# Kernel tuning notes

Measured on AMD Instinct MI355X. Metric: run time of the kernel, lower is better.

Reference implementation:

```python
import jax, jax.numpy as jnp
import numpy as np

B, S, D_IN, D_OUT = 4, 2048, 1024, 1024


def setup_inputs() -> dict:
    key = jax.random.key(0)
    kx, kq, kk, kv = jax.random.split(key, 4)
    scale = 1.0 / np.sqrt(D_IN)
    return {
        "x": jax.random.normal(kx, (B, S, D_IN), dtype=jnp.float32),
        "W_q": jax.random.normal(kq, (D_IN, D_OUT), dtype=jnp.float32) * scale,
        "W_k": jax.random.normal(kk, (D_IN, D_OUT), dtype=jnp.float32) * scale,
        "W_v": jax.random.normal(kv, (D_IN, D_OUT), dtype=jnp.float32) * scale,
    }


def reference(x, W_q, W_k, W_v):
    # QKV projections (Linear without bias): [B,S,D_out]
    q = jnp.einsum("bsd,de->bse", x, W_q)
    k = jnp.einsum("bsd,de->bse", x, W_k)
    v = jnp.einsum("bsd,de->bse", x, W_v)

    # Raw scores [B,S,S], causal mask (strict upper triangle -> -inf),
    # then scale by sqrt(d_k) and softmax, matching the torch order of ops.
    scores = jnp.einsum("bqd,bkd->bqk", q, k)
    seq = scores.shape[-1]
    causal = jnp.triu(jnp.ones((seq, seq), dtype=bool), k=1)
    scores = jnp.where(causal[None, :, :], -jnp.inf, scores)
    attn = jax.nn.softmax(scores / jnp.sqrt(jnp.asarray(q.shape[-1], scores.dtype)), axis=-1)
    # dropout p=0.0 -> identity (eval semantics)
    return jnp.einsum("bqk,bkd->bqd", attn, v)
```

## Files before the change

### kernel.cpp

```cpp
#include <hip/hip_runtime.h>

typedef unsigned short u16;
typedef __bf16 bf16x8 __attribute__((ext_vector_type(8)));
typedef float f32x4 __attribute__((ext_vector_type(4)));

__device__ __forceinline__ u16 f2bf(float f) {
    union { float f; unsigned int u; } v; v.f = f;
    unsigned int u = v.u;
    return (u16)((u + 0x7FFFu + ((u >> 16) & 1u)) >> 16);
}

__device__ __forceinline__ void load_lds16(const void* g, void* l) {
    __builtin_amdgcn_global_load_lds(
        (const __attribute__((address_space(1))) unsigned int*)g,
        (__attribute__((address_space(3))) unsigned int*)l,
        16, 0, 0);
}

__global__ void __launch_bounds__(256) prep_kernel(
    const float4* __restrict__ X, u16* __restrict__ xb,
    const float* __restrict__ Wq, const float* __restrict__ Wk,
    const float* __restrict__ Wv,
    u16* __restrict__ Oq, u16* __restrict__ Ok, u16* __restrict__ Ov,
    float* __restrict__ rowsum) {
    __shared__ float tile[32][33];
    const int bid = blockIdx.x, tid = threadIdx.x;
    if (bid < 8192) {
        int idx = bid * 256 + tid;
        float4 v = X[idx];
        ushort4 o;
        o.x = f2bf(v.x); o.y = f2bf(v.y); o.z = f2bf(v.z); o.w = f2bf(v.w);
        *(ushort4*)(xb + (size_t)idx * 4) = o;
    } else if (bid < 11264) {
        int id = bid - 8192;
        int zz = id >> 10;
        const float* W = (zz == 0) ? Wq : (zz == 1) ? Wk : Wv;
        u16* O = (zz == 0) ? Oq : (zz == 1) ? Ok : Ov;
        int n0 = (id & 31) * 32, k0 = ((id >> 5) & 31) * 32;
        int tx = tid & 31, ty = tid >> 5;
        #pragma unroll
        for (int j = 0; j < 32; j += 8)
            tile[ty + j][tx] = W[(size_t)(k0 + ty + j) * 1024 + n0 + tx];
        __syncthreads();
        #pragma unroll
        for (int j = 0; j < 32; j += 8)
            O[(size_t)(n0 + ty + j) * 1024 + k0 + tx] = f2bf(tile[tx][ty + j]);
    } else {
        rowsum[(bid - 11264) * 256 + tid] = 0.f;
    }
}

template <int MODE>
__global__ void __launch_bounds__(512) gemm_nt(
    const u16* __restrict__ xb, const u16* __restrict__ WqT,
    const u16* __restrict__ WkT, const u16* __restrict__ WvT,
    u16* __restrict__ Q, u16* __restrict__ Kb,
    u16* __restrict__ Vt, u16* __restrict__ S,
    float* __restrict__ rowsum, float* __restrict__ out) {

    int mtile, ntile, z, kiters;
    const u16 *A, *B;

    if (MODE == 0) {
        int L = blockIdx.x;
        int xcd = L & 7;
        int u = L >> 3;
        z = u >> 5;
        int v = u & 31;
        mtile = ((v >> 3) << 3) | xcd;
        ntile = v & 7;
        A = xb;
        B = (z == 0) ? WqT : (z == 1) ? WkT : WvT;
        kiters = 16;
    } else if (MODE == 1) {
        int L = blockIdx.x;
        z = L >> 7;
        int w = L & 127;
        mtile = w >> 4;
        ntile = w & 15;
        if (ntile > 2 * mtile + 1) return;
        A = Q  + (size_t)z * (2048 * 1024);
        B = Kb + (size_t)z * (2048 * 1024);
        kiters = 16;
    } else {
        int L = blockIdx.x;
        ntile = L & 7;
        int mt = L >> 3;
        z = mt >> 3;
        mtile = mt & 7;
        A = S  + (size_t)z * (2048 * 2048);
        B = Vt + (size_t)z * (1024 * 2048);
        kiters = 4 * (mtile + 1);
    }

    const int LDA = (MODE == 2) ? 2048 : 1024;

    __shared__ __align__(16) u16 As[32768];
    __shared__ __align__(16) u16 Bs[16384 + MODE * 128];

    const int tid  = threadIdx.x;
    const int lane = tid & 63;
    const int wave = tid >> 6;
    const int wr = wave >> 1, wc = wave & 1;

    const int r0 = tid >> 2;
    const int kb = (((tid & 3) ^ ((r0 >> 1) & 3))) * 16;

    const char* gA0 = (const char*)(A + (size_t)(mtile * 256 +       r0) * LDA) + kb;
    const char* gA1 = (const char*)(A + (size_t)(mtile * 256 + 128 + r0) * LDA) + kb;
    const char* gB  = (const char*)(B + (size_t)(ntile * 128 +       r0) * LDA) + kb;

    auto STAGE = [&](int buf, int kt) {
        const size_t off = (size_t)kt * 128;
        char* a = (char*)As + buf * 32768 + tid * 16;
        char* b = (char*)Bs + buf * 16384 + tid * 16;
        load_lds16(gA0 + off,      a);
        load_lds16(gA0 + off + 64, a + 8192);
        load_lds16(gA1 + off,      a + 16384);
        load_lds16(gA1 + off + 64, a + 24576);
        load_lds16(gB  + off,      b);
        load_lds16(gB  + off + 64, b + 8192);
    };

    const int quad = lane >> 4;
    const int l16  = lane & 15;
    const int ch   = quad ^ ((l16 >> 1) & 3);
    const int aoff = (wr >> 1) * 8192 + ((wr & 1) * 64 + l16) * 32 + ch * 8;
    const int boff = (wc * 64 + l16) * 32 + ch * 8;

    f32x4 acc[4][4] = {};

    STAGE(0, 0);
    STAGE(1, 1);
    asm volatile("s_waitcnt vmcnt(6)" ::: "memory");
    __builtin_amdgcn_s_barrier();

    int cur = 0;
    for (int kt = 0; kt < kiters; ++kt) {
        const u16* ap = As + cur * 16384 + aoff;
        const u16* bp = Bs + cur * 8192  + boff;
        bf16x8 af[2][4], bv[2][4];
        #pragma unroll
        for (int h = 0; h < 2; ++h) {
            #pragma unroll
            for (int r = 0; r < 4; ++r) af[h][r] = *(const bf16x8*)(ap + h * 4096 + r * 512);
            #pragma unroll
            for (int c = 0; c < 4; ++c) bv[h][c] = *(const bf16x8*)(bp + h * 4096 + c * 512);
        }
        asm volatile("s_waitcnt lgkmcnt(0)" ::: "memory");
        __builtin_amdgcn_sched_barrier(0);
        __builtin_amdgcn_s_barrier();
        if (kt + 2 < kiters) STAGE(cur, kt + 2);

        #pragma unroll
        for (int h = 0; h < 2; ++h)
            #pragma unroll
            for (int r = 0; r < 4; ++r)
                #pragma unroll
                for (int c = 0; c < 4; ++c)
                    acc[r][c] = __builtin_amdgcn_mfma_f32_16x16x32_bf16(
                        af[h][r], bv[h][c], acc[r][c], 0, 0, 0);

        if (kt + 2 < kiters) {
            asm volatile("s_waitcnt vmcnt(6)" ::: "memory");
        } else {
            asm volatile("s_waitcnt vmcnt(0)" ::: "memory");
        }
        __builtin_amdgcn_s_barrier();
        cur ^= 1;
    }

    const int grow0 = mtile * 256 + wr * 64 + quad * 4;
    const int gcol0 = ntile * 128 + wc * 64 + l16;

    if (MODE == 0) {
        if (z < 2) {
            u16* C = z ? Kb : Q;
            #pragma unroll
            for (int r = 0; r < 4; ++r)
                #pragma unroll
                for (int c = 0; c < 4; ++c)
                    #pragma unroll
                    for (int i = 0; i < 4; ++i)
                        C[(size_t)(grow0 + r * 16 + i) * 1024 + gcol0 + c * 16] =
                            f2bf(acc[r][c][i]);
        } else {
            #pragma unroll
            for (int r = 0; r < 4; ++r) {
                int m0 = grow0 + r * 16;
                int b = m0 >> 11, s0 = m0 & 2047;
                #pragma unroll
                for (int c = 0; c < 4; ++c) {
                    int d = gcol0 + c * 16;
                    ushort4 o;
                    o.x = f2bf(acc[r][c][0]); o.y = f2bf(acc[r][c][1]);
                    o.z = f2bf(acc[r][c][2]); o.w = f2bf(acc[r][c][3]);
                    *(ushort4*)(Vt + (size_t)b * (1024 * 2048) + (size_t)d * 2048 + s0) = o;
                }
            }
        }
    } else if (MODE == 1) {
        u16* C = S + (size_t)z * (2048 * 2048);
        float* rs = rowsum + z * 2048;
        const bool maskchk = (ntile >= 2 * mtile);
        float rsum[4][4];
        #pragma unroll
        for (int r = 0; r < 4; ++r)
            #pragma unroll
            for (int i = 0; i < 4; ++i) rsum[r][i] = 0.f;
        #pragma unroll
        for (int r = 0; r < 4; ++r)
            #pragma unroll
            for (int c = 0; c < 4; ++c)
                #pragma unroll
                for (int i = 0; i < 4; ++i) {
                    int grow = grow0 + r * 16 + i;
                    int gcol = gcol0 + c * 16;
                    float e = 0.f;
                    if (!maskchk || gcol <= grow)
                        e = __expf(acc[r][c][i] * 0.03125f - 12.0f);
                    C[(size_t)grow * 2048 + gcol] = f2bf(e);
                    rsum[r][i] += e;
                }
        #pragma unroll
        for (int r = 0; r < 4; ++r)
            #pragma unroll
            for (int i = 0; i < 4; ++i) {
                float s = rsum[r][i];
                s += __shfl_xor(s, 1, 64);
                s += __shfl_xor(s, 2, 64);
                s += __shfl_xor(s, 4, 64);
                s += __shfl_xor(s, 8, 64);
                if (l16 == 0)
                    unsafeAtomicAdd(&rs[grow0 + r * 16 + i], s);
            }
    } else {
        const float* rs = rowsum + z * 2048;
        float* C = out + (size_t)z * (2048 * 1024);
        #pragma unroll
        for (int r = 0; r < 4; ++r)
            #pragma unroll
            for (int i = 0; i < 4; ++i) {
                int grow = grow0 + r * 16 + i;
                float inv = 1.0f / rs[grow];
                #pragma unroll
                for (int c = 0; c < 4; ++c)
                    C[(size_t)grow * 1024 + gcol0 + c * 16] = acc[r][c][i] * inv;
            }
    }
}

extern "C" void kernel_launch(void* const* d_in, const int* in_sizes, int n_in,
                              void* d_out, int out_size, void* d_ws, size_t ws_size,
                              hipStream_t stream) {
    const float* x  = (const float*)d_in[0];
    const float* Wq = (const float*)d_in[1];
    const float* Wk = (const float*)d_in[2];
    const float* Wv = (const float*)d_in[3];
    float* out = (float*)d_out;
    char* ws = (char*)d_ws;
    const size_t Mi = 1u << 20;

    u16* xb  = (u16*)(ws);
    u16* WqT = (u16*)(ws + 16 * Mi);
    u16* WkT = (u16*)(ws + 18 * Mi);
    u16* WvT = (u16*)(ws + 20 * Mi);
    u16* Q   = (u16*)(ws + 22 * Mi);
    u16* Kb  = (u16*)(ws + 38 * Mi);
    u16* Vt  = (u16*)(ws + 54 * Mi);
    u16* S   = (u16*)(ws + 70 * Mi);
    float* rowsum = (float*)(ws + 102 * Mi);

    prep_kernel<<<11296, 256, 0, stream>>>(
        (const float4*)x, xb, Wq, Wk, Wv, WqT, WkT, WvT, rowsum);

    gemm_nt<0><<<768, 512, 0, stream>>>(xb, WqT, WkT, WvT, Q, Kb, Vt, S, rowsum, out);

    gemm_nt<1><<<512, 512, 0, stream>>>(xb, WqT, WkT, WvT, Q, Kb, Vt, S, rowsum, out);

    gemm_nt<2><<<256, 512, 0, stream>>>(xb, WqT, WkT, WvT, Q, Kb, Vt, S, rowsum, out);
}
```

Before: 232.7 us.

## Split-K heavy PV tiles into halves and software-pipeline LDS fragment loads

The PV GEMM (mode 2) used one block per output tile, with K length growing with mtile, so the causal workload was badly imbalanced. The longest row tiles (mtile 5-7) are now split into two K halves. One half writes unnormalized partials to a scratch buffer that reuses the xb region, and a new combine kernel sums the halves and applies the row normalization. The main loop is also restructured to double-buffer LDS fragment reads across k sub-steps, with s_setprio around the MFMA groups, so LDS reads overlap matrix math. This costs an extra kernel launch and extra fp32 global traffic for the partials.

```diff
diff --git a/kernel.cpp b/kernel.cpp
--- a/kernel.cpp
+++ b/kernel.cpp
@@ -16,6 +16,9 @@
         (__attribute__((address_space(3))) unsigned int*)l,
         16, 0, 0);
 }
+
+__constant__ unsigned char cls2_m[11] = {4,7,7,3,6,6,5,5,2,1,0};
+__constant__ unsigned char cls2_h[11] = {2,0,1,2,0,1,0,1,2,2,2};
 
 __global__ void __launch_bounds__(256) prep_kernel(
     const float4* __restrict__ X, u16* __restrict__ xb,
@@ -50,15 +53,35 @@
     }
 }
 
+__global__ void __launch_bounds__(256) combine_kernel(
+    const float4* __restrict__ P1, const float* __restrict__ rowsum,
+    float4* __restrict__ out) {
+    int b = blockIdx.x;
+    int z = b / 768;
+    int lb = b - z * 768;
+    int j = lb * 256 + threadIdx.x;
+    int rl = j >> 8;
+    float inv = 1.0f / rowsum[z * 2048 + 1280 + rl];
+    size_t oi = (size_t)z * 524288 + 327680 + j;
+    float4 a = out[oi];
+    float4 p = P1[(size_t)z * 196608 + j];
+    a.x = (a.x + p.x) * inv;
+    a.y = (a.y + p.y) * inv;
+    a.z = (a.z + p.z) * inv;
+    a.w = (a.w + p.w) * inv;
+    out[oi] = a;
+}
+
 template <int MODE>
 __global__ void __launch_bounds__(512) gemm_nt(
     const u16* __restrict__ xb, const u16* __restrict__ WqT,
     const u16* __restrict__ WkT, const u16* __restrict__ WvT,
     u16* __restrict__ Q, u16* __restrict__ Kb,
     u16* __restrict__ Vt, u16* __restrict__ S,
-    float* __restrict__ rowsum, float* __restrict__ out) {
-
-    int mtile, ntile, z, kiters;
+    float* __restrict__ rowsum, float* __restrict__ out,
+    float* __restrict__ P1) {
+
+    int mtile, ntile, z, kbeg = 0, kiters, kh = 2;
     const u16 *A, *B;
 
     if (MODE == 0) {
@@ -85,12 +108,16 @@
     } else {
         int L = blockIdx.x;
         ntile = L & 7;
-        int mt = L >> 3;
-        z = mt >> 3;
-        mtile = mt & 7;
+        z = (L >> 3) & 3;
+        int ci = L >> 5;
+        mtile = cls2_m[ci];
+        kh = cls2_h[ci];
+        int half = 2 * (mtile + 1);
+        if (kh == 0)      { kbeg = 0;    kiters = half; }
+        else if (kh == 1) { kbeg = half; kiters = half; }
+        else              { kbeg = 0;    kiters = 4 * (mtile + 1); }
         A = S  + (size_t)z * (2048 * 2048);
         B = Vt + (size_t)z * (1024 * 2048);
-        kiters = 4 * (mtile + 1);
     }
 
     const int LDA = (MODE == 2) ? 2048 : 1024;
@@ -106,12 +133,12 @@
     const int r0 = tid >> 2;
     const int kb = (((tid & 3) ^ ((r0 >> 1) & 3))) * 16;
 
-    const char* gA0 = (const char*)(A + (size_t)(mtile * 256 +       r0) * LDA) + kb;
-    const char* gA1 = (const char*)(A + (size_t)(mtile * 256 + 128 + r0) * LDA) + kb;
-    const char* gB  = (const char*)(B + (size_t)(ntile * 128 +       r0) * LDA) + kb;
-
-    auto STAGE = [&](int buf, int kt) {
-        const size_t off = (size_t)kt * 128;
+    const char* gA0 = (const char*)(A + (size_t)(mtile * 256 +       r0) * LDA) + kb + kbeg * 128;
+    const char* gA1 = (const char*)(A + (size_t)(mtile * 256 + 128 + r0) * LDA) + kb + kbeg * 128;
+    const char* gB  = (const char*)(B + (size_t)(ntile * 128 +       r0) * LDA) + kb + kbeg * 128;
+
+    auto STAGE = [&](int buf, int kt2) {
+        const size_t off = (size_t)kt2 * 128;
         char* a = (char*)As + buf * 32768 + tid * 16;
         char* b = (char*)Bs + buf * 16384 + tid * 16;
         load_lds16(gA0 + off,      a);
@@ -129,44 +156,67 @@
     const int boff = (wc * 64 + l16) * 32 + ch * 8;
 
     f32x4 acc[4][4] = {};
+    bf16x8 afA[4], bvA[4], afB[4], bvB[4];
 
     STAGE(0, 0);
     STAGE(1, 1);
     asm volatile("s_waitcnt vmcnt(6)" ::: "memory");
     __builtin_amdgcn_s_barrier();
+    {
+        const u16* ap = As + aoff;
+        const u16* bp = Bs + boff;
+        #pragma unroll
+        for (int r = 0; r < 4; ++r) afA[r] = *(const bf16x8*)(ap + r * 512);
+        #pragma unroll
+        for (int c = 0; c < 4; ++c) bvA[c] = *(const bf16x8*)(bp + c * 512);
+    }
 
     int cur = 0;
     for (int kt = 0; kt < kiters; ++kt) {
-        const u16* ap = As + cur * 16384 + aoff;
-        const u16* bp = Bs + cur * 8192  + boff;
-        bf16x8 af[2][4], bv[2][4];
-        #pragma unroll
-        for (int h = 0; h < 2; ++h) {
-            #pragma unroll
-            for (int r = 0; r < 4; ++r) af[h][r] = *(const bf16x8*)(ap + h * 4096 + r * 512);
-            #pragma unroll
-            for (int c = 0; c < 4; ++c) bv[h][c] = *(const bf16x8*)(bp + h * 4096 + c * 512);
+        {
+            const u16* ap = As + cur * 16384 + 4096 + aoff;
+            const u16* bp = Bs + cur * 8192  + 4096 + boff;
+            #pragma unroll
+            for (int r = 0; r < 4; ++r) afB[r] = *(const bf16x8*)(ap + r * 512);
+            #pragma unroll
+            for (int c = 0; c < 4; ++c) bvB[c] = *(const bf16x8*)(bp + c * 512);
         }
+        asm volatile("s_waitcnt lgkmcnt(8)" ::: "memory");
+        __builtin_amdgcn_sched_barrier(0);
+        __builtin_amdgcn_s_setprio(1);
+        #pragma unroll
+        for (int r = 0; r < 4; ++r)
+            #pragma unroll
+            for (int c = 0; c < 4; ++c)
+                acc[r][c] = __builtin_amdgcn_mfma_f32_16x16x32_bf16(
+                    afA[r], bvA[c], acc[r][c], 0, 0, 0);
+        __builtin_amdgcn_s_setprio(0);
         asm volatile("s_waitcnt lgkmcnt(0)" ::: "memory");
         __builtin_amdgcn_sched_barrier(0);
         __builtin_amdgcn_s_barrier();
         if (kt + 2 < kiters) STAGE(cur, kt + 2);
-
-        #pragma unroll
-        for (int h = 0; h < 2; ++h)
-            #pragma unroll
-            for (int r = 0; r < 4; ++r)
-                #pragma unroll
-                for (int c = 0; c < 4; ++c)
-                    acc[r][c] = __builtin_amdgcn_mfma_f32_16x16x32_bf16(
-                        af[h][r], bv[h][c], acc[r][c], 0, 0, 0);
-
-        if (kt + 2 < kiters) {
-            asm volatile("s_waitcnt vmcnt(6)" ::: "memory");
-        } else {
-            asm volatile("s_waitcnt vmcnt(0)" ::: "memory");
+        if (kt + 1 < kiters) {
+            if (kt + 2 < kiters) {
+                asm volatile("s_waitcnt vmcnt(6)" ::: "memory");
+            } else {
+                asm volatile("s_waitcnt vmcnt(0)" ::: "memory");
+            }
+            __builtin_amdgcn_s_barrier();
+            const u16* ap = As + (cur ^ 1) * 16384 + aoff;
+            const u16* bp = Bs + (cur ^ 1) * 8192  + boff;
+            #pragma unroll
+            for (int r = 0; r < 4; ++r) afA[r] = *(const bf16x8*)(ap + r * 512);
+            #pragma unroll
+            for (int c = 0; c < 4; ++c) bvA[c] = *(const bf16x8*)(bp + c * 512);
         }
-        __builtin_amdgcn_s_barrier();
+        __builtin_amdgcn_s_setprio(1);
+        #pragma unroll
+        for (int r = 0; r < 4; ++r)
+            #pragma unroll
+            for (int c = 0; c < 4; ++c)
+                acc[r][c] = __builtin_amdgcn_mfma_f32_16x16x32_bf16(
+                    afB[r], bvB[c], acc[r][c], 0, 0, 0);
+        __builtin_amdgcn_s_setprio(0);
         cur ^= 1;
     }
 
@@ -235,18 +285,42 @@
                     unsafeAtomicAdd(&rs[grow0 + r * 16 + i], s);
             }
     } else {
-        const float* rs = rowsum + z * 2048;
-        float* C = out + (size_t)z * (2048 * 1024);
-        #pragma unroll
-        for (int r = 0; r < 4; ++r)
-            #pragma unroll
-            for (int i = 0; i < 4; ++i) {
-                int grow = grow0 + r * 16 + i;
-                float inv = 1.0f / rs[grow];
-                #pragma unroll
-                for (int c = 0; c < 4; ++c)
-                    C[(size_t)grow * 1024 + gcol0 + c * 16] = acc[r][c][i] * inv;
-            }
+        if (kh == 2) {
+            const float* rs = rowsum + z * 2048;
+            float* C = out + (size_t)z * (2048 * 1024);
+            #pragma unroll
+            for (int r = 0; r < 4; ++r)
+                #pragma unroll
+                for (int i = 0; i < 4; ++i) {
+                    int grow = grow0 + r * 16 + i;
+                    float inv = 1.0f / rs[grow];
+                    #pragma unroll
+                    for (int c = 0; c < 4; ++c)
+                        C[(size_t)grow * 1024 + gcol0 + c * 16] = acc[r][c][i] * inv;
+                }
+        } else if (kh == 1) {
+            float* C = out + (size_t)z * (2048 * 1024);
+            #pragma unroll
+            for (int r = 0; r < 4; ++r)
+                #pragma unroll
+                for (int i = 0; i < 4; ++i) {
+                    int grow = grow0 + r * 16 + i;
+                    #pragma unroll
+                    for (int c = 0; c < 4; ++c)
+                        C[(size_t)grow * 1024 + gcol0 + c * 16] = acc[r][c][i];
+                }
+        } else {
+            float* Pp = P1 + (size_t)z * (768 * 1024);
+            #pragma unroll
+            for (int r = 0; r < 4; ++r)
+                #pragma unroll
+                for (int i = 0; i < 4; ++i) {
+                    int prow = grow0 + r * 16 + i - 1280;
+                    #pragma unroll
+                    for (int c = 0; c < 4; ++c)
+                        Pp[(size_t)prow * 1024 + gcol0 + c * 16] = acc[r][c][i];
+                }
+        }
     }
 }
 
@@ -270,13 +344,17 @@
     u16* Vt  = (u16*)(ws + 54 * Mi);
     u16* S   = (u16*)(ws + 70 * Mi);
     float* rowsum = (float*)(ws + 102 * Mi);
+    float* P1 = (float*)xb;
 
     prep_kernel<<<11296, 256, 0, stream>>>(
         (const float4*)x, xb, Wq, Wk, Wv, WqT, WkT, WvT, rowsum);
 
-    gemm_nt<0><<<768, 512, 0, stream>>>(xb, WqT, WkT, WvT, Q, Kb, Vt, S, rowsum, out);
-
-    gemm_nt<1><<<512, 512, 0, stream>>>(xb, WqT, WkT, WvT, Q, Kb, Vt, S, rowsum, out);
-
-    gemm_nt<2><<<256, 512, 0, stream>>>(xb, WqT, WkT, WvT, Q, Kb, Vt, S, rowsum, out);
-}
+    gemm_nt<0><<<768, 512, 0, stream>>>(xb, WqT, WkT, WvT, Q, Kb, Vt, S, rowsum, out, P1);
+
+    gemm_nt<1><<<512, 512, 0, stream>>>(xb, WqT, WkT, WvT, Q, Kb, Vt, S, rowsum, out, P1);
+
+    gemm_nt<2><<<352, 512, 0, stream>>>(xb, WqT, WkT, WvT, Q, Kb, Vt, S, rowsum, out, P1);
+
+    combine_kernel<<<3072, 256, 0, stream>>>(
+        (const float4*)P1, rowsum, (float4*)out);
+}
```

Result: slower. 251.1 us (+7.9%).
